# Optimization experiments

Measured on AMD Instinct MI355X. Metric: run time of the kernel, lower is better.

Reference implementation:

```python
import jax, jax.numpy as jnp
import numpy as np

M, T, NX, U = 256, 512, 256, 256


def setup_inputs() -> dict:
    key = jax.random.key(0)
    ks = jax.random.split(key, 8)
    u = lambda k, s: jax.random.uniform(k, s, dtype=jnp.float32) * 0.01
    return {
        "x": jax.random.normal(ks[0], (M, T, NX), dtype=jnp.float32),
        "a0": jax.random.normal(ks[1], (M, U), dtype=jnp.float32),
        "wcx": u(ks[2], (NX, U)),
        "wcc": u(ks[3], (U, U)),
        "bc": jnp.zeros((1, U), jnp.float32),
        "wux": u(ks[4], (NX, U)),
        "wuc": u(ks[5], (U, U)),
        "bu": jnp.zeros((1, U), jnp.float32),
        "wrx": u(ks[6], (NX, U)),
        "wrc": u(ks[7], (U, U)),
        "br": jnp.zeros((1, U), jnp.float32),
    }


def reference(x, a0, wcx, wcc, bc, wux, wuc, bu, wrx, wrc, br):
    # x: [m, t, nx] -> scan over time; state c: [m, units]
    def step(c, xt):
        g_u = jax.nn.sigmoid(c @ wuc + xt @ wux + bu)
        g_r = jax.nn.sigmoid(c @ wrc + xt @ wrx + br)
        # NB: original is (g_r * c_prev) @ wcc due to operator precedence
        cand = jnp.tanh((g_r * c) @ wcc + xt @ wcx + bc)
        c_new = g_u * cand + (1.0 - g_u) * c
        return c_new, None

    c_final, _ = jax.lax.scan(step, a0, jnp.swapaxes(x, 0, 1))
    # return_sequences=False, return_state=False -> last hidden state [m, units]
    return c_final
```

## Files before the change

### kernel.cpp

```cpp
#include <hip/hip_runtime.h>

typedef _Float16 h2 __attribute__((ext_vector_type(2)));
typedef _Float16 h8 __attribute__((ext_vector_type(8)));
typedef float f4v __attribute__((ext_vector_type(4)));

#define U_DIM 256
#define M_DIM 256
#define T_DIM 512

#if defined(__has_builtin)
#if __has_builtin(__builtin_amdgcn_fdot2)
#define HAVE_FDOT2 1
#endif
#endif

__device__ __forceinline__ float fdot2f(h2 a, h2 b, float c) {
#ifdef HAVE_FDOT2
  return __builtin_amdgcn_fdot2(a, b, c, false);
#else
  return fmaf((float)a[0], (float)b[0], fmaf((float)a[1], (float)b[1], c));
#endif
}

__device__ __forceinline__ float fast_sigmoid(float z) {
  return __builtin_amdgcn_rcpf(1.f + __expf(-z));
}
__device__ __forceinline__ float fast_tanh(float z) {
  return fmaf(2.f, __builtin_amdgcn_rcpf(1.f + __expf(-2.f * z)), -1.f);
}

__global__ void conv_x(const float* __restrict__ x, h8* __restrict__ x16, int n8) {
  int i = blockIdx.x * 256 + threadIdx.x;
  if (i >= n8) return;
  const float4* p = (const float4*)(x + (size_t)i * 8);
  float4 v0 = p[0], v1 = p[1];
  h8 o = {(_Float16)v0.x, (_Float16)v0.y, (_Float16)v0.z, (_Float16)v0.w,
          (_Float16)v1.x, (_Float16)v1.y, (_Float16)v1.z, (_Float16)v1.w};
  x16[i] = o;
}

__global__ void prep_xw(const float* __restrict__ wux, const float* __restrict__ wrx,
                        const float* __restrict__ wcx, h8* __restrict__ wt16) {
  int idx = blockIdx.x * 256 + threadIdx.x;
  int mtx = idx >> 13;
  int rem = idx & 8191;
  int n = rem >> 5;
  int kv = rem & 31;
  const float* W = (mtx == 0) ? wux : ((mtx == 1) ? wrx : wcx);
  h8 o;
#pragma unroll
  for (int e = 0; e < 8; ++e) o[e] = (_Float16)W[(size_t)(kv * 8 + e) * U_DIM + n];
  wt16[idx] = o;
}

__global__ void prep_w(const float* __restrict__ wuc, const float* __restrict__ wrc,
                       const float* __restrict__ wcc, h8* __restrict__ w16) {
  int idx = blockIdx.x * 256 + threadIdx.x;
  int mtx = idx >> 13;
  int rem = idx & 8191;
  int tid = rem >> 4;
  int v   = rem & 15;
  int j = tid >> 1, s = tid & 1;
  const float* W = (mtx == 0) ? wuc : ((mtx == 1) ? wrc : wcc);
  int k0 = 128 * s + 8 * v;
  h8 o;
#pragma unroll
  for (int e = 0; e < 8; ++e) o[e] = (_Float16)W[(size_t)(k0 + e) * U_DIM + j];
  w16[idx] = o;
}

__global__ __launch_bounds__(256, 2)
void xproj_mfma(const h8* __restrict__ x16, const h8* __restrict__ wt16,
                const float* __restrict__ Bu, const float* __restrict__ Br,
                const float* __restrict__ Bc,
                float* __restrict__ XU, float* __restrict__ XR, float* __restrict__ XC,
                int t0, int len) {
  const int mtx = blockIdx.z;
  const float* Bv = (mtx == 0) ? Bu : ((mtx == 1) ? Br : Bc);
  float* O = (mtx == 0) ? XU : ((mtx == 1) ? XR : XC);
  const h8* W = wt16 + (size_t)mtx * 256 * 32;

  __shared__ _Float16 a_sh[128][40];
  __shared__ _Float16 b_sh[128][40];

  const int tid = threadIdx.x;
  const int r0 = blockIdx.x * 128;
  const int c0 = blockIdx.y * 128;

  const int srow = tid >> 1;
  const int spart = tid & 1;
  const int r = r0 + srow;
  const int mm = r / len;
  const int tc = r - mm * len;
  const h8* arow = x16 + ((size_t)mm * T_DIM + (size_t)(t0 + tc)) * 32;
  const h8* brow = W + (size_t)(c0 + srow) * 32;

  const int lane = tid & 63;
  const int w = tid >> 6;
  const int quad = lane >> 4;
  const int mrow = lane & 15;

  f4v acc[2][8];
#pragma unroll
  for (int fr = 0; fr < 2; ++fr)
#pragma unroll
    for (int fc = 0; fc < 8; ++fc) acc[fr][fc] = f4v{0.f, 0.f, 0.f, 0.f};

  for (int k8 = 0; k8 < 32; k8 += 4) {
    h8 a0 = arow[k8 + 2 * spart];
    h8 a1 = arow[k8 + 2 * spart + 1];
    h8 b0 = brow[k8 + 2 * spart];
    h8 b1 = brow[k8 + 2 * spart + 1];
    __syncthreads();
    *(h8*)&a_sh[srow][spart * 16]     = a0;
    *(h8*)&a_sh[srow][spart * 16 + 8] = a1;
    *(h8*)&b_sh[srow][spart * 16]     = b0;
    *(h8*)&b_sh[srow][spart * 16 + 8] = b1;
    __syncthreads();
    h8 af0 = *(const h8*)&a_sh[32 * w + mrow][quad * 8];
    h8 af1 = *(const h8*)&a_sh[32 * w + 16 + mrow][quad * 8];
#pragma unroll
    for (int fc = 0; fc < 8; ++fc) {
      h8 bf = *(const h8*)&b_sh[fc * 16 + mrow][quad * 8];
      acc[0][fc] = __builtin_amdgcn_mfma_f32_16x16x32_f16(af0, bf, acc[0][fc], 0, 0, 0);
      acc[1][fc] = __builtin_amdgcn_mfma_f32_16x16x32_f16(af1, bf, acc[1][fc], 0, 0, 0);
    }
  }

#pragma unroll
  for (int fc = 0; fc < 8; ++fc) {
    int col = c0 + fc * 16 + mrow;
    float bb = Bv[col];
#pragma unroll
    for (int fr = 0; fr < 2; ++fr)
#pragma unroll
      for (int reg = 0; reg < 4; ++reg) {
        int rr = r0 + 32 * w + fr * 16 + quad * 4 + reg;
        O[(size_t)rr * U_DIM + col] = acc[fr][fc][reg] + bb;
      }
  }
}

__global__ __launch_bounds__(512, 2)
void gru_rec(const float* __restrict__ XU, const float* __restrict__ XR,
             const float* __restrict__ XC,
             const h8* __restrict__ w16,
             const float* __restrict__ c_in, float* __restrict__ c_out, int len) {
  const int m = blockIdx.x;
  const int tid = threadIdx.x;
  const int j = tid >> 1;
  const int s = tid & 1;
  const int cb = s * 17;
  const int wj = j + ((j >> 7) << 3);

  __shared__ h8 ch8[34];
  __shared__ h8 hh8[34];

  const h8* wub = w16 + (size_t)tid * 16;
  const h8* wrb = wub + 8192;
  const h8* wcb = wub + 16384;

#define DECL_W(i) h8 wu##i = wub[i]; h8 wr##i = wrb[i]; h8 wc##i = wcb[i];
  DECL_W(0)  DECL_W(1)  DECL_W(2)  DECL_W(3)
  DECL_W(4)  DECL_W(5)  DECL_W(6)  DECL_W(7)
  DECL_W(8)  DECL_W(9)  DECL_W(10) DECL_W(11)
  DECL_W(12) DECL_W(13) DECL_W(14) DECL_W(15)
#undef DECL_W

  float cj = c_in[m * U_DIM + j];
  if (s == 0) ((_Float16*)ch8)[wj] = (_Float16)cj;

  const float* XUb = XU + (size_t)m * len * U_DIM;
  const float* XRb = XR + (size_t)m * len * U_DIM;
  const float* XCb = XC + (size_t)m * len * U_DIM;

  int off = j;
  float xuv = XUb[off], xrv = XRb[off], xcv = XCb[off];

  __syncthreads();

  for (int t = 0; t < len; ++t) {
    int offn = off + ((t + 1 < len) ? U_DIM : 0);
    float nxu = XUb[offn], nxr = XRb[offn], nxc = XCb[offn];

    float pu0 = 0.f, pu1 = 0.f, pr0 = 0.f, pr1 = 0.f;
#define PASS1(i) { h8 cv = ch8[cb + i];                                   \
    pu0 = fdot2f(h2{cv[0], cv[1]}, h2{wu##i[0], wu##i[1]}, pu0);          \
    pr0 = fdot2f(h2{cv[0], cv[1]}, h2{wr##i[0], wr##i[1]}, pr0);          \
    pu1 = fdot2f(h2{cv[2], cv[3]}, h2{wu##i[2], wu##i[3]}, pu1);          \
    pr1 = fdot2f(h2{cv[2], cv[3]}, h2{wr##i[2], wr##i[3]}, pr1);          \
    pu0 = fdot2f(h2{cv[4], cv[5]}, h2{wu##i[4], wu##i[5]}, pu0);          \
    pr0 = fdot2f(h2{cv[4], cv[5]}, h2{wr##i[4], wr##i[5]}, pr0);          \
    pu1 = fdot2f(h2{cv[6], cv[7]}, h2{wu##i[6], wu##i[7]}, pu1);          \
    pr1 = fdot2f(h2{cv[6], cv[7]}, h2{wr##i[6], wr##i[7]}, pr1); }
    PASS1(0)  PASS1(1)  PASS1(2)  PASS1(3)
    PASS1(4)  PASS1(5)  PASS1(6)  PASS1(7)
    PASS1(8)  PASS1(9)  PASS1(10) PASS1(11)
    PASS1(12) PASS1(13) PASS1(14) PASS1(15)
#undef PASS1

    float pu = pu0 + pu1;
    pu += __shfl_xor(pu, 1);
    float pr = pr0 + pr1;
    pr += __shfl_xor(pr, 1);

    float gu = fast_sigmoid(pu + xuv);
    float gr = fast_sigmoid(pr + xrv);
    if (s == 0) ((_Float16*)hh8)[wj] = (_Float16)(gr * cj);
    __syncthreads();

    float pc0 = 0.f, pc1 = 0.f;
#define PASS2(i) { h8 hv = hh8[cb + i];                                   \
    pc0 = fdot2f(h2{hv[0], hv[1]}, h2{wc##i[0], wc##i[1]}, pc0);          \
    pc1 = fdot2f(h2{hv[2], hv[3]}, h2{wc##i[2], wc##i[3]}, pc1);          \
    pc0 = fdot2f(h2{hv[4], hv[5]}, h2{wc##i[4], wc##i[5]}, pc0);          \
    pc1 = fdot2f(h2{hv[6], hv[7]}, h2{wc##i[6], wc##i[7]}, pc1); }
    PASS2(0)  PASS2(1)  PASS2(2)  PASS2(3)
    PASS2(4)  PASS2(5)  PASS2(6)  PASS2(7)
    PASS2(8)  PASS2(9)  PASS2(10) PASS2(11)
    PASS2(12) PASS2(13) PASS2(14) PASS2(15)
#undef PASS2

    float pc = pc0 + pc1;
    pc += __shfl_xor(pc, 1);

    float cand = fast_tanh(pc + xcv);
    cj = fmaf(gu, cand - cj, cj);
    if (s == 0) ((_Float16*)ch8)[wj] = (_Float16)cj;

    xuv = nxu; xrv = nxr; xcv = nxc; off = offn;
    __syncthreads();
  }

  if (s == 0) c_out[m * U_DIM + j] = cj;
}

extern "C" void kernel_launch(void* const* d_in, const int* in_sizes, int n_in,
                              void* d_out, int out_size, void* d_ws, size_t ws_size,
                              hipStream_t stream) {
  const float* x   = (const float*)d_in[0];
  const float* a0  = (const float*)d_in[1];
  const float* wcx = (const float*)d_in[2];
  const float* wcc = (const float*)d_in[3];
  const float* bc  = (const float*)d_in[4];
  const float* wux = (const float*)d_in[5];
  const float* wuc = (const float*)d_in[6];
  const float* bu  = (const float*)d_in[7];
  const float* wrx = (const float*)d_in[8];
  const float* wrc = (const float*)d_in[9];
  const float* br  = (const float*)d_in[10];
  float* out = (float*)d_out;

  const size_t x16_bytes = (size_t)M_DIM * T_DIM * U_DIM * 2;
  const size_t wt_bytes  = 3ull * 256 * 32 * 16;
  const size_t w16_bytes = 3ull * 512 * 16 * 16;
  const size_t fixed = x16_bytes + wt_bytes + w16_bytes;

  h8* x16  = (h8*)d_ws;
  h8* wt16 = (h8*)((char*)d_ws + x16_bytes);
  h8* w16  = (h8*)((char*)d_ws + x16_bytes + wt_bytes);
  float* XU0 = (float*)((char*)d_ws + fixed);

  size_t avail = (ws_size > fixed) ? (ws_size - fixed) : 0;
  const size_t perT = 3ull * M_DIM * U_DIM * sizeof(float);
  int Tc = (int)(avail / perT);
  if (Tc > T_DIM) Tc = T_DIM;
  if (Tc < 1) Tc = 1;
  int nch = (T_DIM + Tc - 1) / Tc;
  Tc = (T_DIM + nch - 1) / nch;

  float* XU = XU0;
  float* XR = XU + (size_t)M_DIM * Tc * U_DIM;
  float* XC = XR + (size_t)M_DIM * Tc * U_DIM;

  conv_x<<<16384, 256, 0, stream>>>(x, x16, M_DIM * T_DIM * U_DIM / 8);
  prep_xw<<<96, 256, 0, stream>>>(wux, wrx, wcx, wt16);
  prep_w<<<96, 256, 0, stream>>>(wuc, wrc, wcc, w16);

  for (int t0 = 0; t0 < T_DIM; t0 += Tc) {
    int lenc = (T_DIM - t0) < Tc ? (T_DIM - t0) : Tc;
    dim3 g((M_DIM * lenc) / 128, 2, 3);
    xproj_mfma<<<g, 256, 0, stream>>>(x16, wt16, bu, br, bc,
                                      XU, XR, XC, t0, lenc);
    gru_rec<<<M_DIM, 512, 0, stream>>>(XU, XR, XC, w16,
                                       (t0 == 0 ? a0 : out), out, lenc);
  }
}
```

Before: 1.017 ms.

## Move GRU recurrence to MFMA over 16-row batch tiles, store projections in fp16

The per-step recurrent matmuls move from per-thread fp16 dot2 reductions (one block per batch row) to MFMA 16x16x32 instructions. Each block now handles 16 batch rows, so each weight tile held in registers is reused across the whole tile, and only 16 blocks are launched. The hidden state and gated state are staged in LDS in an MFMA-friendly transposed layout, and the weight prep kernel is rewritten to produce matching fragments. The precomputed input projections are also stored as fp16 instead of fp32, which halves their write and read traffic and allows larger time chunks. The trade-off is much lower GPU occupancy for the sequential recurrence, plus extra rounding in the projections.

```diff
diff --git a/kernel.cpp b/kernel.cpp
--- a/kernel.cpp
+++ b/kernel.cpp
@@ -1,26 +1,13 @@
 #include <hip/hip_runtime.h>
 
 typedef _Float16 h2 __attribute__((ext_vector_type(2)));
+typedef _Float16 h4 __attribute__((ext_vector_type(4)));
 typedef _Float16 h8 __attribute__((ext_vector_type(8)));
 typedef float f4v __attribute__((ext_vector_type(4)));
 
 #define U_DIM 256
 #define M_DIM 256
 #define T_DIM 512
-
-#if defined(__has_builtin)
-#if __has_builtin(__builtin_amdgcn_fdot2)
-#define HAVE_FDOT2 1
-#endif
-#endif
-
-__device__ __forceinline__ float fdot2f(h2 a, h2 b, float c) {
-#ifdef HAVE_FDOT2
-  return __builtin_amdgcn_fdot2(a, b, c, false);
-#else
-  return fmaf((float)a[0], (float)b[0], fmaf((float)a[1], (float)b[1], c));
-#endif
-}
 
 __device__ __forceinline__ float fast_sigmoid(float z) {
   return __builtin_amdgcn_rcpf(1.f + __expf(-z));
@@ -53,31 +40,32 @@
   wt16[idx] = o;
 }
 
-__global__ void prep_w(const float* __restrict__ wuc, const float* __restrict__ wrc,
-                       const float* __restrict__ wcc, h8* __restrict__ w16) {
+__global__ void prep_wa(const float* __restrict__ wuc, const float* __restrict__ wrc,
+                        const float* __restrict__ wcc, h8* __restrict__ wa) {
   int idx = blockIdx.x * 256 + threadIdx.x;
-  int mtx = idx >> 13;
+  int mtx = idx / 8192;
   int rem = idx & 8191;
-  int tid = rem >> 4;
-  int v   = rem & 15;
-  int j = tid >> 1, s = tid & 1;
+  int ut = rem >> 9;
+  int kk = (rem >> 6) & 7;
+  int lane = rem & 63;
   const float* W = (mtx == 0) ? wuc : ((mtx == 1) ? wrc : wcc);
-  int k0 = 128 * s + 8 * v;
+  int u = ut * 16 + (lane & 15);
+  int k0 = kk * 32 + (lane >> 4) * 8;
   h8 o;
 #pragma unroll
-  for (int e = 0; e < 8; ++e) o[e] = (_Float16)W[(size_t)(k0 + e) * U_DIM + j];
-  w16[idx] = o;
+  for (int e = 0; e < 8; ++e) o[e] = (_Float16)W[(size_t)(k0 + e) * U_DIM + u];
+  wa[idx] = o;
 }
 
 __global__ __launch_bounds__(256, 2)
 void xproj_mfma(const h8* __restrict__ x16, const h8* __restrict__ wt16,
                 const float* __restrict__ Bu, const float* __restrict__ Br,
                 const float* __restrict__ Bc,
-                float* __restrict__ XU, float* __restrict__ XR, float* __restrict__ XC,
-                int t0, int len) {
+                _Float16* __restrict__ XU, _Float16* __restrict__ XR,
+                _Float16* __restrict__ XC, int t0, int len) {
   const int mtx = blockIdx.z;
   const float* Bv = (mtx == 0) ? Bu : ((mtx == 1) ? Br : Bc);
-  float* O = (mtx == 0) ? XU : ((mtx == 1) ? XR : XC);
+  _Float16* O = (mtx == 0) ? XU : ((mtx == 1) ? XR : XC);
   const h8* W = wt16 + (size_t)mtx * 256 * 32;
 
   __shared__ _Float16 a_sh[128][40];
@@ -136,103 +124,121 @@
 #pragma unroll
       for (int reg = 0; reg < 4; ++reg) {
         int rr = r0 + 32 * w + fr * 16 + quad * 4 + reg;
-        O[(size_t)rr * U_DIM + col] = acc[fr][fc][reg] + bb;
+        O[(size_t)rr * U_DIM + col] = (_Float16)(acc[fr][fc][reg] + bb);
       }
   }
 }
 
 __global__ __launch_bounds__(512, 2)
-void gru_rec(const float* __restrict__ XU, const float* __restrict__ XR,
-             const float* __restrict__ XC,
-             const h8* __restrict__ w16,
-             const float* __restrict__ c_in, float* __restrict__ c_out, int len) {
-  const int m = blockIdx.x;
+void gru_mfma(const _Float16* __restrict__ XU, const _Float16* __restrict__ XR,
+              const _Float16* __restrict__ XC, const h8* __restrict__ wa,
+              const float* __restrict__ c_in, float* __restrict__ c_out, int len) {
+  const int m0 = blockIdx.x * 16;
   const int tid = threadIdx.x;
-  const int j = tid >> 1;
-  const int s = tid & 1;
-  const int cb = s * 17;
-  const int wj = j + ((j >> 7) << 3);
-
-  __shared__ h8 ch8[34];
-  __shared__ h8 hh8[34];
-
-  const h8* wub = w16 + (size_t)tid * 16;
-  const h8* wrb = wub + 8192;
-  const h8* wcb = wub + 16384;
-
-#define DECL_W(i) h8 wu##i = wub[i]; h8 wr##i = wrb[i]; h8 wc##i = wcb[i];
-  DECL_W(0)  DECL_W(1)  DECL_W(2)  DECL_W(3)
-  DECL_W(4)  DECL_W(5)  DECL_W(6)  DECL_W(7)
-  DECL_W(8)  DECL_W(9)  DECL_W(10) DECL_W(11)
-  DECL_W(12) DECL_W(13) DECL_W(14) DECL_W(15)
-#undef DECL_W
-
-  float cj = c_in[m * U_DIM + j];
-  if (s == 0) ((_Float16*)ch8)[wj] = (_Float16)cj;
-
-  const float* XUb = XU + (size_t)m * len * U_DIM;
-  const float* XRb = XR + (size_t)m * len * U_DIM;
-  const float* XCb = XC + (size_t)m * len * U_DIM;
-
-  int off = j;
-  float xuv = XUb[off], xrv = XRb[off], xcv = XCb[off];
+  const int lane = tid & 63;
+  const int w = tid >> 6;
+  const int quad = lane >> 4;
+  const int n = lane & 15;
+
+  __shared__ h8 ct[512];
+  __shared__ h8 gt[512];
+
+#define DECLW(NM, MI, TI) \
+  h8 NM##_0, NM##_1, NM##_2, NM##_3, NM##_4, NM##_5, NM##_6, NM##_7; \
+  { const h8* p = wa + (size_t)((((MI)*16) + (2*w + (TI))) * 8) * 64 + lane; \
+    NM##_0 = p[0];   NM##_1 = p[64];  NM##_2 = p[128]; NM##_3 = p[192]; \
+    NM##_4 = p[256]; NM##_5 = p[320]; NM##_6 = p[384]; NM##_7 = p[448]; }
+  DECLW(wU0, 0, 0) DECLW(wU1, 0, 1)
+  DECLW(wR0, 1, 0) DECLW(wR1, 1, 1)
+  DECLW(wC0, 2, 0) DECLW(wC1, 2, 1)
+#undef DECLW
+
+  const int u0 = (2 * w) * 16 + quad * 4;
+  const int u1 = u0 + 16;
+
+  f4v cv0 = *(const f4v*)(c_in + (size_t)(m0 + n) * U_DIM + u0);
+  f4v cv1 = *(const f4v*)(c_in + (size_t)(m0 + n) * U_DIM + u1);
+
+  _Float16* cp0 = (_Float16*)ct + ((u0 >> 3) * 16 + n) * 8 + (u0 & 7);
+  _Float16* cp1 = (_Float16*)ct + ((u1 >> 3) * 16 + n) * 8 + (u1 & 7);
+  _Float16* gp0 = (_Float16*)gt + ((u0 >> 3) * 16 + n) * 8 + (u0 & 7);
+  _Float16* gp1 = (_Float16*)gt + ((u1 >> 3) * 16 + n) * 8 + (u1 & 7);
+
+  { h4 t0 = {(_Float16)cv0[0], (_Float16)cv0[1], (_Float16)cv0[2], (_Float16)cv0[3]};
+    h4 t1 = {(_Float16)cv1[0], (_Float16)cv1[1], (_Float16)cv1[2], (_Float16)cv1[3]};
+    *(h4*)cp0 = t0; *(h4*)cp1 = t1; }
+
+  const size_t rowoff = (size_t)(m0 + n) * len * U_DIM;
+  const _Float16* xu0p = XU + rowoff + u0;
+  const _Float16* xu1p = XU + rowoff + u1;
+  const _Float16* xr0p = XR + rowoff + u0;
+  const _Float16* xr1p = XR + rowoff + u1;
+  const _Float16* xc0p = XC + rowoff + u0;
+  const _Float16* xc1p = XC + rowoff + u1;
+
+  h4 xu0 = *(const h4*)xu0p, xu1 = *(const h4*)xu1p;
+  h4 xr0 = *(const h4*)xr0p, xr1 = *(const h4*)xr1p;
+  h4 xc0 = *(const h4*)xc0p, xc1 = *(const h4*)xc1p;
 
   __syncthreads();
 
   for (int t = 0; t < len; ++t) {
-    int offn = off + ((t + 1 < len) ? U_DIM : 0);
-    float nxu = XUb[offn], nxr = XRb[offn], nxc = XCb[offn];
-
-    float pu0 = 0.f, pu1 = 0.f, pr0 = 0.f, pr1 = 0.f;
-#define PASS1(i) { h8 cv = ch8[cb + i];                                   \
-    pu0 = fdot2f(h2{cv[0], cv[1]}, h2{wu##i[0], wu##i[1]}, pu0);          \
-    pr0 = fdot2f(h2{cv[0], cv[1]}, h2{wr##i[0], wr##i[1]}, pr0);          \
-    pu1 = fdot2f(h2{cv[2], cv[3]}, h2{wu##i[2], wu##i[3]}, pu1);          \
-    pr1 = fdot2f(h2{cv[2], cv[3]}, h2{wr##i[2], wr##i[3]}, pr1);          \
-    pu0 = fdot2f(h2{cv[4], cv[5]}, h2{wu##i[4], wu##i[5]}, pu0);          \
-    pr0 = fdot2f(h2{cv[4], cv[5]}, h2{wr##i[4], wr##i[5]}, pr0);          \
-    pu1 = fdot2f(h2{cv[6], cv[7]}, h2{wu##i[6], wu##i[7]}, pu1);          \
-    pr1 = fdot2f(h2{cv[6], cv[7]}, h2{wr##i[6], wr##i[7]}, pr1); }
-    PASS1(0)  PASS1(1)  PASS1(2)  PASS1(3)
-    PASS1(4)  PASS1(5)  PASS1(6)  PASS1(7)
-    PASS1(8)  PASS1(9)  PASS1(10) PASS1(11)
-    PASS1(12) PASS1(13) PASS1(14) PASS1(15)
-#undef PASS1
-
-    float pu = pu0 + pu1;
-    pu += __shfl_xor(pu, 1);
-    float pr = pr0 + pr1;
-    pr += __shfl_xor(pr, 1);
-
-    float gu = fast_sigmoid(pu + xuv);
-    float gr = fast_sigmoid(pr + xrv);
-    if (s == 0) ((_Float16*)hh8)[wj] = (_Float16)(gr * cj);
-    __syncthreads();
-
-    float pc0 = 0.f, pc1 = 0.f;
-#define PASS2(i) { h8 hv = hh8[cb + i];                                   \
-    pc0 = fdot2f(h2{hv[0], hv[1]}, h2{wc##i[0], wc##i[1]}, pc0);          \
-    pc1 = fdot2f(h2{hv[2], hv[3]}, h2{wc##i[2], wc##i[3]}, pc1);          \
-    pc0 = fdot2f(h2{hv[4], hv[5]}, h2{wc##i[4], wc##i[5]}, pc0);          \
-    pc1 = fdot2f(h2{hv[6], hv[7]}, h2{wc##i[6], wc##i[7]}, pc1); }
-    PASS2(0)  PASS2(1)  PASS2(2)  PASS2(3)
-    PASS2(4)  PASS2(5)  PASS2(6)  PASS2(7)
-    PASS2(8)  PASS2(9)  PASS2(10) PASS2(11)
-    PASS2(12) PASS2(13) PASS2(14) PASS2(15)
-#undef PASS2
-
-    float pc = pc0 + pc1;
-    pc += __shfl_xor(pc, 1);
-
-    float cand = fast_tanh(pc + xcv);
-    cj = fmaf(gu, cand - cj, cj);
-    if (s == 0) ((_Float16*)ch8)[wj] = (_Float16)cj;
-
-    xuv = nxu; xrv = nxr; xcv = nxc; off = offn;
-    __syncthreads();
-  }
-
-  if (s == 0) c_out[m * U_DIM + j] = cj;
+    size_t noff = (size_t)((t + 1 < len) ? t + 1 : t) * U_DIM;
+    h4 nxu0 = *(const h4*)(xu0p + noff), nxu1 = *(const h4*)(xu1p + noff);
+    h4 nxr0 = *(const h4*)(xr0p + noff), nxr1 = *(const h4*)(xr1p + noff);
+    h4 nxc0 = *(const h4*)(xc0p + noff), nxc1 = *(const h4*)(xc1p + noff);
+
+    f4v aU0 = {0.f,0.f,0.f,0.f}, aU1 = {0.f,0.f,0.f,0.f};
+    f4v aR0 = {0.f,0.f,0.f,0.f}, aR1 = {0.f,0.f,0.f,0.f};
+#define P1(K) { h8 bf = ct[((K)*4 + quad)*16 + n]; \
+    aU0 = __builtin_amdgcn_mfma_f32_16x16x32_f16(wU0_##K, bf, aU0, 0, 0, 0); \
+    aU1 = __builtin_amdgcn_mfma_f32_16x16x32_f16(wU1_##K, bf, aU1, 0, 0, 0); \
+    aR0 = __builtin_amdgcn_mfma_f32_16x16x32_f16(wR0_##K, bf, aR0, 0, 0, 0); \
+    aR1 = __builtin_amdgcn_mfma_f32_16x16x32_f16(wR1_##K, bf, aR1, 0, 0, 0); }
+    P1(0) P1(1) P1(2) P1(3) P1(4) P1(5) P1(6) P1(7)
+#undef P1
+
+    f4v gu0, gu1;
+    h4 g0, g1;
+#pragma unroll
+    for (int r = 0; r < 4; ++r) {
+      gu0[r] = fast_sigmoid(aU0[r] + (float)xu0[r]);
+      gu1[r] = fast_sigmoid(aU1[r] + (float)xu1[r]);
+      float gr0 = fast_sigmoid(aR0[r] + (float)xr0[r]);
+      float gr1 = fast_sigmoid(aR1[r] + (float)xr1[r]);
+      g0[r] = (_Float16)(gr0 * cv0[r]);
+      g1[r] = (_Float16)(gr1 * cv1[r]);
+    }
+    *(h4*)gp0 = g0;
+    *(h4*)gp1 = g1;
+    __syncthreads();
+
+    f4v aC0 = {0.f,0.f,0.f,0.f}, aC1 = {0.f,0.f,0.f,0.f};
+#define P2(K) { h8 bf = gt[((K)*4 + quad)*16 + n]; \
+    aC0 = __builtin_amdgcn_mfma_f32_16x16x32_f16(wC0_##K, bf, aC0, 0, 0, 0); \
+    aC1 = __builtin_amdgcn_mfma_f32_16x16x32_f16(wC1_##K, bf, aC1, 0, 0, 0); }
+    P2(0) P2(1) P2(2) P2(3) P2(4) P2(5) P2(6) P2(7)
+#undef P2
+
+    h4 c0h, c1h;
+#pragma unroll
+    for (int r = 0; r < 4; ++r) {
+      float cand0 = fast_tanh(aC0[r] + (float)xc0[r]);
+      float cand1 = fast_tanh(aC1[r] + (float)xc1[r]);
+      cv0[r] = fmaf(gu0[r], cand0 - cv0[r], cv0[r]);
+      cv1[r] = fmaf(gu1[r], cand1 - cv1[r], cv1[r]);
+      c0h[r] = (_Float16)cv0[r];
+      c1h[r] = (_Float16)cv1[r];
+    }
+    *(h4*)cp0 = c0h;
+    *(h4*)cp1 = c1h;
+
+    xu0 = nxu0; xu1 = nxu1; xr0 = nxr0; xr1 = nxr1; xc0 = nxc0; xc1 = nxc1;
+    __syncthreads();
+  }
+
+  *(f4v*)(c_out + (size_t)(m0 + n) * U_DIM + u0) = cv0;
+  *(f4v*)(c_out + (size_t)(m0 + n) * U_DIM + u1) = cv1;
 }
 
 extern "C" void kernel_launch(void* const* d_in, const int* in_sizes, int n_in,
@@ -253,36 +259,36 @@
 
   const size_t x16_bytes = (size_t)M_DIM * T_DIM * U_DIM * 2;
   const size_t wt_bytes  = 3ull * 256 * 32 * 16;
-  const size_t w16_bytes = 3ull * 512 * 16 * 16;
-  const size_t fixed = x16_bytes + wt_bytes + w16_bytes;
+  const size_t wa_bytes  = 3ull * 16 * 8 * 64 * 16;
+  const size_t fixed = x16_bytes + wt_bytes + wa_bytes;
 
   h8* x16  = (h8*)d_ws;
   h8* wt16 = (h8*)((char*)d_ws + x16_bytes);
-  h8* w16  = (h8*)((char*)d_ws + x16_bytes + wt_bytes);
-  float* XU0 = (float*)((char*)d_ws + fixed);
+  h8* wa   = (h8*)((char*)d_ws + x16_bytes + wt_bytes);
+  _Float16* XU0 = (_Float16*)((char*)d_ws + fixed);
 
   size_t avail = (ws_size > fixed) ? (ws_size - fixed) : 0;
-  const size_t perT = 3ull * M_DIM * U_DIM * sizeof(float);
+  const size_t perT = 3ull * M_DIM * U_DIM * 2;
   int Tc = (int)(avail / perT);
   if (Tc > T_DIM) Tc = T_DIM;
   if (Tc < 1) Tc = 1;
   int nch = (T_DIM + Tc - 1) / Tc;
   Tc = (T_DIM + nch - 1) / nch;
 
-  float* XU = XU0;
-  float* XR = XU + (size_t)M_DIM * Tc * U_DIM;
-  float* XC = XR + (size_t)M_DIM * Tc * U_DIM;
+  _Float16* XU = XU0;
+  _Float16* XR = XU + (size_t)M_DIM * Tc * U_DIM;
+  _Float16* XC = XR + (size_t)M_DIM * Tc * U_DIM;
 
   conv_x<<<16384, 256, 0, stream>>>(x, x16, M_DIM * T_DIM * U_DIM / 8);
   prep_xw<<<96, 256, 0, stream>>>(wux, wrx, wcx, wt16);
-  prep_w<<<96, 256, 0, stream>>>(wuc, wrc, wcc, w16);
+  prep_wa<<<96, 256, 0, stream>>>(wuc, wrc, wcc, wa);
 
   for (int t0 = 0; t0 < T_DIM; t0 += Tc) {
     int lenc = (T_DIM - t0) < Tc ? (T_DIM - t0) : Tc;
     dim3 g((M_DIM * lenc) / 128, 2, 3);
     xproj_mfma<<<g, 256, 0, stream>>>(x16, wt16, bu, br, bc,
                                       XU, XR, XC, t0, lenc);
-    gru_rec<<<M_DIM, 512, 0, stream>>>(XU, XR, XC, w16,
-                                       (t0 == 0 ? a0 : out), out, lenc);
-  }
-}
+    gru_mfma<<<16, 512, 0, stream>>>(XU, XR, XC, wa,
+                                     (t0 == 0 ? a0 : out), out, lenc);
+  }
+}
```

Result: slower. 1.514 ms (+48.9%).

## Store gate projections in fp16 and remap recurrence to 8-way K split with 4 units/group

Applied to the files above, without the earlier changes.

The x-projection outputs XU/XR/XC are now written and read as fp16 instead of fp32, halving that intermediate traffic and allowing larger time chunks in the workspace. The recurrent kernel is reorganised so each group of 8 threads owns 4 output units and splits the K dimension 8 ways. Each thread reuses one loaded state vector across 4 units, partial sums are combined with a 3-step shuffle reduction, and the shared-memory layout is padded against bank conflicts. This costs extra shuffles, leaves only one lane in eight doing the gate math, and adds fp16 rounding of the precomputed gate inputs.

```diff
diff --git a/kernel.cpp b/kernel.cpp
--- a/kernel.cpp
+++ b/kernel.cpp
@@ -1,6 +1,7 @@
 #include <hip/hip_runtime.h>
 
 typedef _Float16 h2 __attribute__((ext_vector_type(2)));
+typedef _Float16 h4 __attribute__((ext_vector_type(4)));
 typedef _Float16 h8 __attribute__((ext_vector_type(8)));
 typedef float f4v __attribute__((ext_vector_type(4)));
 
@@ -27,6 +28,12 @@
 }
 __device__ __forceinline__ float fast_tanh(float z) {
   return fmaf(2.f, __builtin_amdgcn_rcpf(1.f + __expf(-2.f * z)), -1.f);
+}
+__device__ __forceinline__ float red8(float v) {
+  v += __shfl_xor(v, 1);
+  v += __shfl_xor(v, 2);
+  v += __shfl_xor(v, 4);
+  return v;
 }
 
 __global__ void conv_x(const float* __restrict__ x, h8* __restrict__ x16, int n8) {
@@ -53,31 +60,33 @@
   wt16[idx] = o;
 }
 
-__global__ void prep_w(const float* __restrict__ wuc, const float* __restrict__ wrc,
-                       const float* __restrict__ wcc, h8* __restrict__ w16) {
+__global__ void prep_w48(const float* __restrict__ wuc, const float* __restrict__ wrc,
+                         const float* __restrict__ wcc, h8* __restrict__ w48) {
   int idx = blockIdx.x * 256 + threadIdx.x;
-  int mtx = idx >> 13;
-  int rem = idx & 8191;
-  int tid = rem >> 4;
-  int v   = rem & 15;
-  int j = tid >> 1, s = tid & 1;
+  int slot = idx >> 9;
+  int tid = idx & 511;
+  int mtx = slot >> 4;
+  int uu = (slot >> 2) & 3;
+  int cc = slot & 3;
+  int g = tid >> 3, sp = tid & 7;
   const float* W = (mtx == 0) ? wuc : ((mtx == 1) ? wrc : wcc);
-  int k0 = 128 * s + 8 * v;
+  int j = 4 * g + uu;
+  int k0 = 32 * sp + 8 * cc;
   h8 o;
 #pragma unroll
   for (int e = 0; e < 8; ++e) o[e] = (_Float16)W[(size_t)(k0 + e) * U_DIM + j];
-  w16[idx] = o;
+  w48[idx] = o;
 }
 
 __global__ __launch_bounds__(256, 2)
 void xproj_mfma(const h8* __restrict__ x16, const h8* __restrict__ wt16,
                 const float* __restrict__ Bu, const float* __restrict__ Br,
                 const float* __restrict__ Bc,
-                float* __restrict__ XU, float* __restrict__ XR, float* __restrict__ XC,
-                int t0, int len) {
+                _Float16* __restrict__ XU, _Float16* __restrict__ XR,
+                _Float16* __restrict__ XC, int t0, int len) {
   const int mtx = blockIdx.z;
   const float* Bv = (mtx == 0) ? Bu : ((mtx == 1) ? Br : Bc);
-  float* O = (mtx == 0) ? XU : ((mtx == 1) ? XR : XC);
+  _Float16* O = (mtx == 0) ? XU : ((mtx == 1) ? XR : XC);
   const h8* W = wt16 + (size_t)mtx * 256 * 32;
 
   __shared__ _Float16 a_sh[128][40];
@@ -136,103 +145,122 @@
 #pragma unroll
       for (int reg = 0; reg < 4; ++reg) {
         int rr = r0 + 32 * w + fr * 16 + quad * 4 + reg;
-        O[(size_t)rr * U_DIM + col] = acc[fr][fc][reg] + bb;
+        O[(size_t)rr * U_DIM + col] = (_Float16)(acc[fr][fc][reg] + bb);
       }
   }
 }
 
 __global__ __launch_bounds__(512, 2)
-void gru_rec(const float* __restrict__ XU, const float* __restrict__ XR,
-             const float* __restrict__ XC,
-             const h8* __restrict__ w16,
+void gru_rec(const _Float16* __restrict__ XU, const _Float16* __restrict__ XR,
+             const _Float16* __restrict__ XC, const h8* __restrict__ w48,
              const float* __restrict__ c_in, float* __restrict__ c_out, int len) {
   const int m = blockIdx.x;
   const int tid = threadIdx.x;
-  const int j = tid >> 1;
-  const int s = tid & 1;
-  const int cb = s * 17;
-  const int wj = j + ((j >> 7) << 3);
-
-  __shared__ h8 ch8[34];
-  __shared__ h8 hh8[34];
-
-  const h8* wub = w16 + (size_t)tid * 16;
-  const h8* wrb = wub + 8192;
-  const h8* wcb = wub + 16384;
-
-#define DECL_W(i) h8 wu##i = wub[i]; h8 wr##i = wrb[i]; h8 wc##i = wcb[i];
-  DECL_W(0)  DECL_W(1)  DECL_W(2)  DECL_W(3)
-  DECL_W(4)  DECL_W(5)  DECL_W(6)  DECL_W(7)
-  DECL_W(8)  DECL_W(9)  DECL_W(10) DECL_W(11)
-  DECL_W(12) DECL_W(13) DECL_W(14) DECL_W(15)
-#undef DECL_W
-
-  float cj = c_in[m * U_DIM + j];
-  if (s == 0) ((_Float16*)ch8)[wj] = (_Float16)cj;
-
-  const float* XUb = XU + (size_t)m * len * U_DIM;
-  const float* XRb = XR + (size_t)m * len * U_DIM;
-  const float* XCb = XC + (size_t)m * len * U_DIM;
-
-  int off = j;
-  float xuv = XUb[off], xrv = XRb[off], xcv = XCb[off];
+  const int g = tid >> 3;
+  const int sp = tid & 7;
+  const bool sp0 = (sp == 0);
+
+  __shared__ h8 ct[40];
+  __shared__ h8 gt[40];
+
+#define DECLW3(uu, cc) \
+  h8 wU##uu##cc = w48[(size_t)((0 * 4 + uu) * 4 + cc) * 512 + tid]; \
+  h8 wR##uu##cc = w48[(size_t)((1 * 4 + uu) * 4 + cc) * 512 + tid]; \
+  h8 wC##uu##cc = w48[(size_t)((2 * 4 + uu) * 4 + cc) * 512 + tid];
+  DECLW3(0, 0) DECLW3(0, 1) DECLW3(0, 2) DECLW3(0, 3)
+  DECLW3(1, 0) DECLW3(1, 1) DECLW3(1, 2) DECLW3(1, 3)
+  DECLW3(2, 0) DECLW3(2, 1) DECLW3(2, 2) DECLW3(2, 3)
+  DECLW3(3, 0) DECLW3(3, 1) DECLW3(3, 2) DECLW3(3, 3)
+#undef DECLW3
+
+  const int pc0 = (g >> 1) + (g >> 3);
+  _Float16* cslot = (_Float16*)ct + pc0 * 8 + (g & 1) * 4;
+  _Float16* gslot = (_Float16*)gt + pc0 * 8 + (g & 1) * 4;
+
+  f4v cj = *(const f4v*)(c_in + (size_t)m * U_DIM + 4 * g);
+  if (sp0) {
+    h4 c0h = {(_Float16)cj[0], (_Float16)cj[1], (_Float16)cj[2], (_Float16)cj[3]};
+    *(h4*)cslot = c0h;
+  }
+
+  const size_t rowbase = (size_t)m * len * U_DIM + 4 * g;
+  const _Float16* xup = XU + rowbase;
+  const _Float16* xrp = XR + rowbase;
+  const _Float16* xcp = XC + rowbase;
+
+  h4 xu = *(const h4*)xup, xr = *(const h4*)xrp, xc = *(const h4*)xcp;
 
   __syncthreads();
 
   for (int t = 0; t < len; ++t) {
-    int offn = off + ((t + 1 < len) ? U_DIM : 0);
-    float nxu = XUb[offn], nxr = XRb[offn], nxc = XCb[offn];
-
-    float pu0 = 0.f, pu1 = 0.f, pr0 = 0.f, pr1 = 0.f;
-#define PASS1(i) { h8 cv = ch8[cb + i];                                   \
-    pu0 = fdot2f(h2{cv[0], cv[1]}, h2{wu##i[0], wu##i[1]}, pu0);          \
-    pr0 = fdot2f(h2{cv[0], cv[1]}, h2{wr##i[0], wr##i[1]}, pr0);          \
-    pu1 = fdot2f(h2{cv[2], cv[3]}, h2{wu##i[2], wu##i[3]}, pu1);          \
-    pr1 = fdot2f(h2{cv[2], cv[3]}, h2{wr##i[2], wr##i[3]}, pr1);          \
-    pu0 = fdot2f(h2{cv[4], cv[5]}, h2{wu##i[4], wu##i[5]}, pu0);          \
-    pr0 = fdot2f(h2{cv[4], cv[5]}, h2{wr##i[4], wr##i[5]}, pr0);          \
-    pu1 = fdot2f(h2{cv[6], cv[7]}, h2{wu##i[6], wu##i[7]}, pu1);          \
-    pr1 = fdot2f(h2{cv[6], cv[7]}, h2{wr##i[6], wr##i[7]}, pr1); }
-    PASS1(0)  PASS1(1)  PASS1(2)  PASS1(3)
-    PASS1(4)  PASS1(5)  PASS1(6)  PASS1(7)
-    PASS1(8)  PASS1(9)  PASS1(10) PASS1(11)
-    PASS1(12) PASS1(13) PASS1(14) PASS1(15)
-#undef PASS1
-
-    float pu = pu0 + pu1;
-    pu += __shfl_xor(pu, 1);
-    float pr = pr0 + pr1;
-    pr += __shfl_xor(pr, 1);
-
-    float gu = fast_sigmoid(pu + xuv);
-    float gr = fast_sigmoid(pr + xrv);
-    if (s == 0) ((_Float16*)hh8)[wj] = (_Float16)(gr * cj);
+    size_t noff = (size_t)((t + 1 < len) ? t + 1 : t) * U_DIM;
+    h4 nxu = *(const h4*)(xup + noff);
+    h4 nxr = *(const h4*)(xrp + noff);
+    h4 nxc = *(const h4*)(xcp + noff);
+
+#define D8(acc, wv, cv) \
+    acc = fdot2f(h2{cv[0], cv[1]}, h2{wv[0], wv[1]}, acc); \
+    acc = fdot2f(h2{cv[2], cv[3]}, h2{wv[2], wv[3]}, acc); \
+    acc = fdot2f(h2{cv[4], cv[5]}, h2{wv[4], wv[5]}, acc); \
+    acc = fdot2f(h2{cv[6], cv[7]}, h2{wv[6], wv[7]}, acc);
+
+    float pu0 = 0.f, pu1 = 0.f, pu2 = 0.f, pu3 = 0.f;
+    float pr0 = 0.f, pr1 = 0.f, pr2 = 0.f, pr3 = 0.f;
+#define P1C(cc) { h8 cv = ct[5 * sp + cc]; \
+    D8(pu0, wU0##cc, cv) D8(pr0, wR0##cc, cv) \
+    D8(pu1, wU1##cc, cv) D8(pr1, wR1##cc, cv) \
+    D8(pu2, wU2##cc, cv) D8(pr2, wR2##cc, cv) \
+    D8(pu3, wU3##cc, cv) D8(pr3, wR3##cc, cv) }
+    P1C(0) P1C(1) P1C(2) P1C(3)
+#undef P1C
+
+    pu0 = red8(pu0); pu1 = red8(pu1); pu2 = red8(pu2); pu3 = red8(pu3);
+    pr0 = red8(pr0); pr1 = red8(pr1); pr2 = red8(pr2); pr3 = red8(pr3);
+
+    f4v gu;
+    if (sp0) {
+      gu[0] = fast_sigmoid(pu0 + (float)xu[0]);
+      gu[1] = fast_sigmoid(pu1 + (float)xu[1]);
+      gu[2] = fast_sigmoid(pu2 + (float)xu[2]);
+      gu[3] = fast_sigmoid(pu3 + (float)xu[3]);
+      float gr0 = fast_sigmoid(pr0 + (float)xr[0]);
+      float gr1 = fast_sigmoid(pr1 + (float)xr[1]);
+      float gr2 = fast_sigmoid(pr2 + (float)xr[2]);
+      float gr3 = fast_sigmoid(pr3 + (float)xr[3]);
+      h4 gh = {(_Float16)(gr0 * cj[0]), (_Float16)(gr1 * cj[1]),
+               (_Float16)(gr2 * cj[2]), (_Float16)(gr3 * cj[3])};
+      *(h4*)gslot = gh;
+    }
     __syncthreads();
 
-    float pc0 = 0.f, pc1 = 0.f;
-#define PASS2(i) { h8 hv = hh8[cb + i];                                   \
-    pc0 = fdot2f(h2{hv[0], hv[1]}, h2{wc##i[0], wc##i[1]}, pc0);          \
-    pc1 = fdot2f(h2{hv[2], hv[3]}, h2{wc##i[2], wc##i[3]}, pc1);          \
-    pc0 = fdot2f(h2{hv[4], hv[5]}, h2{wc##i[4], wc##i[5]}, pc0);          \
-    pc1 = fdot2f(h2{hv[6], hv[7]}, h2{wc##i[6], wc##i[7]}, pc1); }
-    PASS2(0)  PASS2(1)  PASS2(2)  PASS2(3)
-    PASS2(4)  PASS2(5)  PASS2(6)  PASS2(7)
-    PASS2(8)  PASS2(9)  PASS2(10) PASS2(11)
-    PASS2(12) PASS2(13) PASS2(14) PASS2(15)
-#undef PASS2
-
-    float pc = pc0 + pc1;
-    pc += __shfl_xor(pc, 1);
-
-    float cand = fast_tanh(pc + xcv);
-    cj = fmaf(gu, cand - cj, cj);
-    if (s == 0) ((_Float16*)ch8)[wj] = (_Float16)cj;
-
-    xuv = nxu; xrv = nxr; xcv = nxc; off = offn;
+    float pc0 = 0.f, pc1 = 0.f, pc2 = 0.f, pc3 = 0.f;
+#define P2C(cc) { h8 hv = gt[5 * sp + cc]; \
+    D8(pc0, wC0##cc, hv) D8(pc1, wC1##cc, hv) \
+    D8(pc2, wC2##cc, hv) D8(pc3, wC3##cc, hv) }
+    P2C(0) P2C(1) P2C(2) P2C(3)
+#undef P2C
+#undef D8
+
+    pc0 = red8(pc0); pc1 = red8(pc1); pc2 = red8(pc2); pc3 = red8(pc3);
+
+    if (sp0) {
+      float cand0 = fast_tanh(pc0 + (float)xc[0]);
+      float cand1 = fast_tanh(pc1 + (float)xc[1]);
+      float cand2 = fast_tanh(pc2 + (float)xc[2]);
+      float cand3 = fast_tanh(pc3 + (float)xc[3]);
+      cj[0] = fmaf(gu[0], cand0 - cj[0], cj[0]);
+      cj[1] = fmaf(gu[1], cand1 - cj[1], cj[1]);
+      cj[2] = fmaf(gu[2], cand2 - cj[2], cj[2]);
+      cj[3] = fmaf(gu[3], cand3 - cj[3], cj[3]);
+      h4 ch = {(_Float16)cj[0], (_Float16)cj[1], (_Float16)cj[2], (_Float16)cj[3]};
+      *(h4*)cslot = ch;
+    }
+
+    xu = nxu; xr = nxr; xc = nxc;
     __syncthreads();
   }
 
-  if (s == 0) c_out[m * U_DIM + j] = cj;
+  if (sp0) *(f4v*)(c_out + (size_t)m * U_DIM + 4 * g) = cj;
 }
 
 extern "C" void kernel_launch(void* const* d_in, const int* in_sizes, int n_in,
@@ -253,36 +281,36 @@
 
   const size_t x16_bytes = (size_t)M_DIM * T_DIM * U_DIM * 2;
   const size_t wt_bytes  = 3ull * 256 * 32 * 16;
-  const size_t w16_bytes = 3ull * 512 * 16 * 16;
-  const size_t fixed = x16_bytes + wt_bytes + w16_bytes;
+  const size_t w48_bytes = 48ull * 512 * 16;
+  const size_t fixed = x16_bytes + wt_bytes + w48_bytes;
 
   h8* x16  = (h8*)d_ws;
   h8* wt16 = (h8*)((char*)d_ws + x16_bytes);
-  h8* w16  = (h8*)((char*)d_ws + x16_bytes + wt_bytes);
-  float* XU0 = (float*)((char*)d_ws + fixed);
+  h8* w48  = (h8*)((char*)d_ws + x16_bytes + wt_bytes);
+  _Float16* XU0 = (_Float16*)((char*)d_ws + fixed);
 
   size_t avail = (ws_size > fixed) ? (ws_size - fixed) : 0;
-  const size_t perT = 3ull * M_DIM * U_DIM * sizeof(float);
+  const size_t perT = 3ull * M_DIM * U_DIM * 2;
   int Tc = (int)(avail / perT);
   if (Tc > T_DIM) Tc = T_DIM;
   if (Tc < 1) Tc = 1;
   int nch = (T_DIM + Tc - 1) / Tc;
   Tc = (T_DIM + nch - 1) / nch;
 
-  float* XU = XU0;
-  float* XR = XU + (size_t)M_DIM * Tc * U_DIM;
-  float* XC = XR + (size_t)M_DIM * Tc * U_DIM;
+  _Float16* XU = XU0;
+  _Float16* XR = XU + (size_t)M_DIM * Tc * U_DIM;
+  _Float16* XC = XR + (size_t)M_DIM * Tc * U_DIM;
 
   conv_x<<<16384, 256, 0, stream>>>(x, x16, M_DIM * T_DIM * U_DIM / 8);
   prep_xw<<<96, 256, 0, stream>>>(wux, wrx, wcx, wt16);
-  prep_w<<<96, 256, 0, stream>>>(wuc, wrc, wcc, w16);
+  prep_w48<<<96, 256, 0, stream>>>(wuc, wrc, wcc, w48);
 
   for (int t0 = 0; t0 < T_DIM; t0 += Tc) {
     int lenc = (T_DIM - t0) < Tc ? (T_DIM - t0) : Tc;
     dim3 g((M_DIM * lenc) / 128, 2, 3);
     xproj_mfma<<<g, 256, 0, stream>>>(x16, wt16, bu, br, bc,
                                       XU, XR, XC, t0, lenc);
-    gru_rec<<<M_DIM, 512, 0, stream>>>(XU, XR, XC, w16,
+    gru_rec<<<M_DIM, 512, 0, stream>>>(XU, XR, XC, w48,
                                        (t0 == 0 ? a0 : out), out, lenc);
   }
 }
```

Result: slower. 1.279 ms (+25.8%).
